# Performance work log

Hardware: AMD Instinct MI355X
Metric: run time of the kernel (lower is better)

The kernel has to match this reference:

```python
import jax, jax.numpy as jnp
from jax import lax
import numpy as np

N = 262144   # occupied voxels
C = 128      # channels
D = 96
K = 27       # 3x3x3 kernel offsets


def _build_kernel_map():
    """Random sparse voxel set + per-offset neighbor indices (Minkowski kernel map)."""
    rng = np.random.default_rng(0)
    cand = rng.integers(0, D, size=(4 * N, 3))
    flat = cand[:, 0] * D * D + cand[:, 1] * D + cand[:, 2]
    uniq = np.unique(flat)[:N]  # N unique occupied voxels
    coords = np.stack([uniq // (D * D), (uniq // D) % D, uniq % D], axis=1)
    lookup = np.full(D * D * D, -1, np.int32)
    lookup[uniq] = np.arange(N, dtype=np.int32)
    offs = np.stack(np.meshgrid([-1, 0, 1], [-1, 0, 1], [-1, 0, 1], indexing='ij'), -1).reshape(-1, 3)
    nc = coords[:, None, :] + offs[None, :, :]            # [N,27,3]
    inb = np.all((nc >= 0) & (nc < D), axis=-1)           # in-bounds
    ncc = np.clip(nc, 0, D - 1)
    nflat = ncc[..., 0] * D * D + ncc[..., 1] * D + ncc[..., 2]
    nid = lookup[nflat]
    mask = inb & (nid >= 0)
    nbr = np.where(mask, nid, 0).astype(np.int32)
    return jnp.asarray(nbr), jnp.asarray(mask)


def setup_inputs() -> dict:
    nbr, mask = _build_kernel_map()
    key = jax.random.key(0)
    ks = jax.random.split(key, 7)
    C4, C2 = C // 4, C // 2
    s3 = lambda cin: 1.0 / np.sqrt(K * cin)
    s1 = lambda cin: 1.0 / np.sqrt(cin)
    return {
        'x':   jax.random.normal(ks[0], (N, C), jnp.float32),
        'nbr': nbr,
        'mask': mask,
        'W00': jax.random.normal(ks[1], (K, C, C4), jnp.float32) * s3(C),
        'b00': jnp.zeros((C4,), jnp.float32),
        'W01': jax.random.normal(ks[2], (K, C4, C2), jnp.float32) * s3(C4),
        'b01': jnp.zeros((C2,), jnp.float32),
        'W10': jax.random.normal(ks[3], (C, C4), jnp.float32) * s1(C),
        'b10': jnp.zeros((C4,), jnp.float32),
        'W11': jax.random.normal(ks[4], (K, C4, C4), jnp.float32) * s3(C4),
        'b11': jnp.zeros((C4,), jnp.float32),
        'W12': jax.random.normal(ks[5], (C4, C2), jnp.float32) * s1(C4),
        'b12': jnp.zeros((C2,), jnp.float32),
    }


def _sparse_conv3(x, W, b, nbr_t, mask_t):
    """Minkowski 3x3x3 stride-1 conv: gather-GEMM-accumulate per kernel offset.
    x: [N,Cin], W: [27,Cin,Cout], nbr_t/mask_t: [27,N]."""
    acc0 = jnp.zeros((x.shape[0], W.shape[-1]), x.dtype)
    def step(acc, kin):
        Wk, idx, m = kin
        return acc + (x[idx] * m[:, None]) @ Wk, None
    y, _ = lax.scan(step, acc0, (W, nbr_t, mask_t))
    return y + b


def reference(x, nbr, mask, W00, b00, W01, b01, W10, b10, W11, b11, W12, b12):
    nbr_t = nbr.T                       # [27,N]
    mask_t = mask.T.astype(x.dtype)     # [27,N]
    # branch 0: conv3x3 -> relu -> conv3x3
    t = jax.nn.relu(_sparse_conv3(x, W00, b00, nbr_t, mask_t))
    out0 = _sparse_conv3(t, W01, b01, nbr_t, mask_t)
    # branch 1: conv1x1 -> relu -> conv3x3 -> relu -> conv1x1
    u = jax.nn.relu(x @ W10 + b10)
    u = jax.nn.relu(_sparse_conv3(u, W11, b11, nbr_t, mask_t))
    out1 = u @ W12 + b12
    # ME.cat(out0, out1) + x  (features concat on channel dim, residual add)
    return jnp.concatenate([out0, out1], axis=1) + x
```

## Files before the change

### kernel.cpp

```cpp
#include <hip/hip_runtime.h>
#include <stdint.h>

#define NVOX 262144
#define CIN  128
#define KOFF 27

typedef short  bf16x8 __attribute__((ext_vector_type(8)));
typedef float  f32x4  __attribute__((ext_vector_type(4)));
typedef int    i32x4  __attribute__((ext_vector_type(4)));

__device__ __forceinline__ unsigned short f2bf(float x) {
    unsigned int u = __builtin_bit_cast(unsigned int, x);
    u += 0x7fff + ((u >> 16) & 1);
    return (unsigned short)(u >> 16);
}

__global__ void k_detect(const int* __restrict__ mask_i32, int* __restrict__ flag) {
    bool ok = true;
    for (int i = threadIdx.x; i < 256; i += 64) {
        int v = mask_i32[i];
        ok = ok && (v == 0 || v == 1);
    }
    unsigned long long b = __ballot(ok);
    if (threadIdx.x == 0) *flag = (b == ~0ull) ? 1 : 0;
}

__device__ __forceinline__ void pack_one(const float* __restrict__ W,
                                         unsigned short* __restrict__ out,
                                         int K, int Nc, int idx) {
    int j    = idx & 7;
    int lane = (idx >> 3) & 63;
    int f    = idx >> 9;
    int ntiles = Nc >> 4, kcs = K >> 5;
    int g  = f / (kcs * ntiles);
    int rem = f - g * (kcs * ntiles);
    int kc = rem / ntiles;
    int nt = rem - kc * ntiles;
    int k  = kc * 32 + ((lane >> 4) << 3) + j;
    int n  = nt * 16 + (lane & 15);
    out[idx] = f2bf(W[((size_t)g * K + k) * Nc + n]);
}

#define PREP_R0 6912
#define PREP_R1 23296
#define PREP_GRID 24076

__global__ __launch_bounds__(256) void k_prep(
    const int* __restrict__ nbr, const void* __restrict__ mask,
    const int* __restrict__ flag, int* __restrict__ nbr_eff,
    const float* __restrict__ x, uint4* __restrict__ xb,
    const float* __restrict__ W00, const float* __restrict__ W10,
    const float* __restrict__ W01, const float* __restrict__ W11,
    const float* __restrict__ W12,
    unsigned short* __restrict__ w00p, unsigned short* __restrict__ w10p,
    unsigned short* __restrict__ w01p, unsigned short* __restrict__ w11p,
    unsigned short* __restrict__ w12p)
{
    int b = blockIdx.x, tid = threadIdx.x;
    if (b < PREP_R0) {
        int base = (b * 256 + tid) * 4;
        i32x4 nv = *(const i32x4*)(nbr + base);
        i32x4 r;
        if (*flag) {
            i32x4 mv = *(const i32x4*)((const int*)mask + base);
            r.x = mv.x ? nv.x : -1;
            r.y = mv.y ? nv.y : -1;
            r.z = mv.z ? nv.z : -1;
            r.w = mv.w ? nv.w : -1;
        } else {
            uchar4 mv = *(const uchar4*)((const unsigned char*)mask + base);
            r.x = mv.x ? nv.x : -1;
            r.y = mv.y ? nv.y : -1;
            r.z = mv.z ? nv.z : -1;
            r.w = mv.w ? nv.w : -1;
        }
        *(i32x4*)(nbr_eff + base) = r;
    } else if (b < PREP_R1) {
        int i = (b - PREP_R0) * 256 + tid;
        const float4* p = (const float4*)x + (size_t)i * 2;
        float4 a = p[0], c = p[1];
        uint4 r;
        r.x = f2bf(a.x) | ((unsigned)f2bf(a.y) << 16);
        r.y = f2bf(a.z) | ((unsigned)f2bf(a.w) << 16);
        r.z = f2bf(c.x) | ((unsigned)f2bf(c.y) << 16);
        r.w = f2bf(c.z) | ((unsigned)f2bf(c.w) << 16);
        xb[i] = r;
    } else {
        int idx = (b - PREP_R1) * 256 + tid;
        if      (idx < 110592) pack_one(W00, w00p, 128, 32, idx);
        else if (idx < 114688) pack_one(W10, w10p, 128, 32, idx - 110592);
        else if (idx < 169984) pack_one(W01, w01p,  32, 64, idx - 114688);
        else if (idx < 197632) pack_one(W11, w11p,  32, 32, idx - 169984);
        else                   pack_one(W12, w12p,  32, 64, idx - 197632);
    }
}

__global__ __launch_bounds__(256) void k_convA(
    const unsigned short* __restrict__ xb,
    const int* __restrict__ nbr_eff,
    const unsigned short* __restrict__ w00, const unsigned short* __restrict__ w10,
    const float* __restrict__ b00, const float* __restrict__ b10,
    unsigned short* __restrict__ s_out)
{
    __shared__ alignas(16) int nbr_s[128 * 27];
    __shared__ unsigned short stage[128 * 72];

    int tid = threadIdx.x;
    int lb = ((blockIdx.x & 7) << 8) | (blockIdx.x >> 3);
    int vb = lb * 128;
    {
        const i32x4* nsrc = (const i32x4*)(nbr_eff + (size_t)vb * 27);
        for (int i = tid; i < 864; i += 256)
            ((i32x4*)nbr_s)[i] = __builtin_nontemporal_load(nsrc + i);
    }
    __syncthreads();

    int lane = tid & 63, wave = tid >> 6;
    int m = lane & 15, q = lane >> 4;
    int vl0 = wave * 32 + m, vl1 = vl0 + 16;

    const bf16x8 zero = {0,0,0,0,0,0,0,0};
    f32x4 zz = {0.f,0.f,0.f,0.f};
    f32x4 t00 = zz, t01 = zz, t10 = zz, t11 = zz;
    f32x4 u00 = zz, u01 = zz, u10 = zz, u11 = zz;

#pragma unroll
    for (int ko = 0; ko < 27; ++ko) {
        int j0 = nbr_s[vl0 * 27 + ko];
        int j1 = nbr_s[vl1 * 27 + ko];
        bool m0 = j0 >= 0, m1 = j1 >= 0;
        const bf16x8* xr0 = (const bf16x8*)(xb + (size_t)(m0 ? j0 : 0) * 128 + q * 8);
        const bf16x8* xr1 = (const bf16x8*)(xb + (size_t)(m1 ? j1 : 0) * 128 + q * 8);
        bf16x8 a0[4], a1[4];
#pragma unroll
        for (int kc = 0; kc < 4; ++kc) {
            a0[kc] = m0 ? xr0[kc * 4] : zero;
            a1[kc] = m1 ? xr1[kc * 4] : zero;
        }
        const bf16x8* wp = (const bf16x8*)(w00) + (size_t)ko * 8 * 64 + lane;
        __builtin_amdgcn_s_setprio(1);
#pragma unroll
        for (int kc = 0; kc < 4; ++kc) {
            bf16x8 bb0 = wp[kc * 128];
            bf16x8 bb1 = wp[kc * 128 + 64];
            t00 = __builtin_amdgcn_mfma_f32_16x16x32_bf16(a0[kc], bb0, t00, 0, 0, 0);
            t01 = __builtin_amdgcn_mfma_f32_16x16x32_bf16(a0[kc], bb1, t01, 0, 0, 0);
            t10 = __builtin_amdgcn_mfma_f32_16x16x32_bf16(a1[kc], bb0, t10, 0, 0, 0);
            t11 = __builtin_amdgcn_mfma_f32_16x16x32_bf16(a1[kc], bb1, t11, 0, 0, 0);
        }
        __builtin_amdgcn_s_setprio(0);
        if (ko == 13) {
            const bf16x8* wq = (const bf16x8*)(w10) + lane;
            __builtin_amdgcn_s_setprio(1);
#pragma unroll
            for (int kc = 0; kc < 4; ++kc) {
                bf16x8 c0 = wq[kc * 128];
                bf16x8 c1 = wq[kc * 128 + 64];
                u00 = __builtin_amdgcn_mfma_f32_16x16x32_bf16(a0[kc], c0, u00, 0, 0, 0);
                u01 = __builtin_amdgcn_mfma_f32_16x16x32_bf16(a0[kc], c1, u01, 0, 0, 0);
                u10 = __builtin_amdgcn_mfma_f32_16x16x32_bf16(a1[kc], c0, u10, 0, 0, 0);
                u11 = __builtin_amdgcn_mfma_f32_16x16x32_bf16(a1[kc], c1, u11, 0, 0, 0);
            }
            __builtin_amdgcn_s_setprio(0);
        }
    }

    int col = lane & 15;
    float bt0 = b00[col], bt1 = b00[16 + col];
    float bu0 = b10[col], bu1 = b10[16 + col];
#pragma unroll
    for (int r = 0; r < 4; ++r) {
        int row0 = wave * 32 + q * 4 + r;
        unsigned short* sp0 = stage + row0 * 72;
        sp0[col]      = f2bf(fmaxf(t00[r] + bt0, 0.f));
        sp0[16 + col] = f2bf(fmaxf(t01[r] + bt1, 0.f));
        sp0[32 + col] = f2bf(fmaxf(u00[r] + bu0, 0.f));
        sp0[48 + col] = f2bf(fmaxf(u01[r] + bu1, 0.f));
        unsigned short* sp1 = sp0 + 16 * 72;
        sp1[col]      = f2bf(fmaxf(t10[r] + bt0, 0.f));
        sp1[16 + col] = f2bf(fmaxf(t11[r] + bt1, 0.f));
        sp1[32 + col] = f2bf(fmaxf(u10[r] + bu0, 0.f));
        sp1[48 + col] = f2bf(fmaxf(u11[r] + bu1, 0.f));
    }
    __syncthreads();
    uint4* g4 = (uint4*)(s_out + (size_t)vb * 64);
    for (int i = tid; i < 1024; i += 256) {
        int row = i >> 3, c = i & 7;
        g4[row * 8 + c] = *(const uint4*)(stage + row * 72 + c * 8);
    }
}

__global__ __launch_bounds__(256) void k_convB(
    const unsigned short* __restrict__ s_in,
    const float* __restrict__ x,
    const int* __restrict__ nbr_eff,
    const unsigned short* __restrict__ w01, const unsigned short* __restrict__ w11,
    const unsigned short* __restrict__ w12,
    const float* __restrict__ b01, const float* __restrict__ b11,
    const float* __restrict__ b12,
    float* __restrict__ out)
{
    __shared__ alignas(16) int nbr_s[128 * 27];
    __shared__ unsigned short vstage[4][2][16 * 40];

    int tid = threadIdx.x;
    int lb = ((blockIdx.x & 7) << 8) | (blockIdx.x >> 3);
    int vb = lb * 128;
    {
        const i32x4* nsrc = (const i32x4*)(nbr_eff + (size_t)vb * 27);
        for (int i = tid; i < 864; i += 256)
            ((i32x4*)nbr_s)[i] = __builtin_nontemporal_load(nsrc + i);
    }
    __syncthreads();

    int lane = tid & 63, wave = tid >> 6;
    int m = lane & 15, q = lane >> 4;
    int vl0 = wave * 32 + m, vl1 = vl0 + 16;

    const bf16x8 zero = {0,0,0,0,0,0,0,0};
    f32x4 zz = {0.f,0.f,0.f,0.f};
    f32x4 o[2][4];
    f32x4 v[2][2];
#pragma unroll
    for (int tl = 0; tl < 2; ++tl) {
        o[tl][0] = zz; o[tl][1] = zz; o[tl][2] = zz; o[tl][3] = zz;
        v[tl][0] = zz; v[tl][1] = zz;
    }

#pragma unroll
    for (int ko = 0; ko < 27; ++ko) {
        int j0 = nbr_s[vl0 * 27 + ko];
        int j1 = nbr_s[vl1 * 27 + ko];
        bool m0 = j0 >= 0, m1 = j1 >= 0;
        const bf16x8* sr0 = (const bf16x8*)(s_in + (size_t)(m0 ? j0 : 0) * 64 + q * 8);
        const bf16x8* sr1 = (const bf16x8*)(s_in + (size_t)(m1 ? j1 : 0) * 64 + q * 8);
        bf16x8 at0 = m0 ? sr0[0] : zero;
        bf16x8 au0 = m0 ? sr0[4] : zero;
        bf16x8 at1 = m1 ? sr1[0] : zero;
        bf16x8 au1 = m1 ? sr1[4] : zero;
        const bf16x8* wp1 = (const bf16x8*)(w01) + (size_t)ko * 4 * 64 + lane;
        __builtin_amdgcn_s_setprio(1);
#pragma unroll
        for (int nt = 0; nt < 4; ++nt) {
            bf16x8 bb = wp1[nt * 64];
            o[0][nt] = __builtin_amdgcn_mfma_f32_16x16x32_bf16(at0, bb, o[0][nt], 0, 0, 0);
            o[1][nt] = __builtin_amdgcn_mfma_f32_16x16x32_bf16(at1, bb, o[1][nt], 0, 0, 0);
        }
        const bf16x8* wp2 = (const bf16x8*)(w11) + (size_t)ko * 2 * 64 + lane;
#pragma unroll
        for (int nt = 0; nt < 2; ++nt) {
            bf16x8 bb = wp2[nt * 64];
            v[0][nt] = __builtin_amdgcn_mfma_f32_16x16x32_bf16(au0, bb, v[0][nt], 0, 0, 0);
            v[1][nt] = __builtin_amdgcn_mfma_f32_16x16x32_bf16(au1, bb, v[1][nt], 0, 0, 0);
        }
        __builtin_amdgcn_s_setprio(0);
    }

    int col = lane & 15;
    {
        float bv0 = b11[col], bv1 = b11[16 + col];
#pragma unroll
        for (int tl = 0; tl < 2; ++tl) {
            unsigned short* vs = vstage[wave][tl];
#pragma unroll
            for (int r = 0; r < 4; ++r) {
                int row = q * 4 + r;
                vs[row * 40 + col]      = f2bf(fmaxf(v[tl][0][r] + bv0, 0.f));
                vs[row * 40 + 16 + col] = f2bf(fmaxf(v[tl][1][r] + bv1, 0.f));
            }
        }
    }
    __syncthreads();
    const bf16x8* wp3 = (const bf16x8*)(w12) + lane;
    bf16x8 w3[4];
#pragma unroll
    for (int nt = 0; nt < 4; ++nt) w3[nt] = wp3[nt * 64];
    f32x4 p[2][4];
#pragma unroll
    for (int tl = 0; tl < 2; ++tl) {
        bf16x8 av = *(const bf16x8*)(vstage[wave][tl] + m * 40 + q * 8);
#pragma unroll
        for (int nt = 0; nt < 4; ++nt)
            p[tl][nt] = __builtin_amdgcn_mfma_f32_16x16x32_bf16(av, w3[nt], zz, 0, 0, 0);
    }

    float bo[4], bp[4];
#pragma unroll
    for (int nt = 0; nt < 4; ++nt) { bo[nt] = b01[nt * 16 + col]; bp[nt] = b12[nt * 16 + col]; }
#pragma unroll
    for (int tl = 0; tl < 2; ++tl) {
#pragma unroll
        for (int r = 0; r < 4; ++r) {
            int row = vb + wave * 32 + tl * 16 + q * 4 + r;
            const float* xr = x + (size_t)row * 128;
            float* orow = out + (size_t)row * 128;
#pragma unroll
            for (int nt = 0; nt < 4; ++nt) {
                float x0 = __builtin_nontemporal_load(xr + nt * 16 + col);
                float x1 = __builtin_nontemporal_load(xr + 64 + nt * 16 + col);
                __builtin_nontemporal_store(o[tl][nt][r] + bo[nt] + x0,
                                            orow + nt * 16 + col);
                __builtin_nontemporal_store(p[tl][nt][r] + bp[nt] + x1,
                                            orow + 64 + nt * 16 + col);
            }
        }
    }
}

extern "C" void kernel_launch(void* const* d_in, const int* in_sizes, int n_in,
                              void* d_out, int out_size, void* d_ws, size_t ws_size,
                              hipStream_t stream) {
    const float* x   = (const float*)d_in[0];
    const int*   nbr = (const int*)d_in[1];
    const void*  mask = d_in[2];
    const float* W00 = (const float*)d_in[3];
    const float* b00 = (const float*)d_in[4];
    const float* W01 = (const float*)d_in[5];
    const float* b01 = (const float*)d_in[6];
    const float* W10 = (const float*)d_in[7];
    const float* b10 = (const float*)d_in[8];
    const float* W11 = (const float*)d_in[9];
    const float* b11 = (const float*)d_in[10];
    const float* W12 = (const float*)d_in[11];
    const float* b12 = (const float*)d_in[12];
    float* out = (float*)d_out;

    char* ws = (char*)d_ws;
    unsigned short* xb     = (unsigned short*)(ws);
    unsigned short* s      = (unsigned short*)(ws + 67108864);
    int*            nbr_eff= (int*)           (ws + 100663296);
    unsigned short* w00p   = (unsigned short*)(ws + 128974848);
    unsigned short* w10p   = (unsigned short*)(ws + 129196032);
    unsigned short* w01p   = (unsigned short*)(ws + 129204224);
    unsigned short* w11p   = (unsigned short*)(ws + 129314816);
    unsigned short* w12p   = (unsigned short*)(ws + 129370112);
    int*            flag   = (int*)           (ws + 129374208);

    k_detect<<<1, 64, 0, stream>>>((const int*)mask, flag);
    k_prep<<<PREP_GRID, 256, 0, stream>>>(nbr, mask, flag, nbr_eff, x, (uint4*)xb,
                                          W00, W10, W01, W11, W12,
                                          w00p, w10p, w01p, w11p, w12p);
    k_convA<<<NVOX/128, 256, 0, stream>>>(xb, nbr_eff, w00p, w10p, b00, b10, s);
    k_convB<<<NVOX/128, 256, 0, stream>>>(s, x, nbr_eff, w01p, w11p, w12p,
                                          b01, b11, b12, out);
}
```

Baseline: 647.3 us.

## Cut register and LDS pressure in conv kernels to raise occupancy

k_convB now processes its two 16-voxel tiles one after another instead of together, which halves the live accumulators and the vstage LDS buffer. Launch-bounds hints ask for 8 and 6 waves per SIMD. k_convA reuses one LDS allocation for both the neighbour table and the output stage, with an added barrier between the two uses. k_prep switches its streaming loads to nontemporal ones. The aim is more waves in flight to hide gather latency, at the cost of less independent MFMA work per wave and possible register spills.

```diff
diff --git a/kernel.cpp b/kernel.cpp
--- a/kernel.cpp
+++ b/kernel.cpp
@@ -5,9 +5,10 @@
 #define CIN  128
 #define KOFF 27
 
-typedef short  bf16x8 __attribute__((ext_vector_type(8)));
-typedef float  f32x4  __attribute__((ext_vector_type(4)));
-typedef int    i32x4  __attribute__((ext_vector_type(4)));
+typedef short        bf16x8 __attribute__((ext_vector_type(8)));
+typedef float        f32x4  __attribute__((ext_vector_type(4)));
+typedef int          i32x4  __attribute__((ext_vector_type(4)));
+typedef unsigned int u32x4  __attribute__((ext_vector_type(4)));
 
 __device__ __forceinline__ unsigned short f2bf(float x) {
     unsigned int u = __builtin_bit_cast(unsigned int, x);
@@ -48,7 +49,7 @@
 __global__ __launch_bounds__(256) void k_prep(
     const int* __restrict__ nbr, const void* __restrict__ mask,
     const int* __restrict__ flag, int* __restrict__ nbr_eff,
-    const float* __restrict__ x, uint4* __restrict__ xb,
+    const float* __restrict__ x, u32x4* __restrict__ xb,
     const float* __restrict__ W00, const float* __restrict__ W10,
     const float* __restrict__ W01, const float* __restrict__ W11,
     const float* __restrict__ W12,
@@ -59,27 +60,29 @@
     int b = blockIdx.x, tid = threadIdx.x;
     if (b < PREP_R0) {
         int base = (b * 256 + tid) * 4;
-        i32x4 nv = *(const i32x4*)(nbr + base);
+        i32x4 nv = __builtin_nontemporal_load((const i32x4*)(nbr + base));
         i32x4 r;
         if (*flag) {
-            i32x4 mv = *(const i32x4*)((const int*)mask + base);
+            i32x4 mv = __builtin_nontemporal_load((const i32x4*)((const int*)mask + base));
             r.x = mv.x ? nv.x : -1;
             r.y = mv.y ? nv.y : -1;
             r.z = mv.z ? nv.z : -1;
             r.w = mv.w ? nv.w : -1;
         } else {
-            uchar4 mv = *(const uchar4*)((const unsigned char*)mask + base);
-            r.x = mv.x ? nv.x : -1;
-            r.y = mv.y ? nv.y : -1;
-            r.z = mv.z ? nv.z : -1;
-            r.w = mv.w ? nv.w : -1;
+            unsigned int mv = __builtin_nontemporal_load(
+                (const unsigned int*)((const unsigned char*)mask + base));
+            r.x = (mv & 0x000000ffu) ? nv.x : -1;
+            r.y = (mv & 0x0000ff00u) ? nv.y : -1;
+            r.z = (mv & 0x00ff0000u) ? nv.z : -1;
+            r.w = (mv & 0xff000000u) ? nv.w : -1;
         }
         *(i32x4*)(nbr_eff + base) = r;
     } else if (b < PREP_R1) {
         int i = (b - PREP_R0) * 256 + tid;
-        const float4* p = (const float4*)x + (size_t)i * 2;
-        float4 a = p[0], c = p[1];
-        uint4 r;
+        const f32x4* p = (const f32x4*)x + (size_t)i * 2;
+        f32x4 a = __builtin_nontemporal_load(p);
+        f32x4 c = __builtin_nontemporal_load(p + 1);
+        u32x4 r;
         r.x = f2bf(a.x) | ((unsigned)f2bf(a.y) << 16);
         r.y = f2bf(a.z) | ((unsigned)f2bf(a.w) << 16);
         r.z = f2bf(c.x) | ((unsigned)f2bf(c.y) << 16);
@@ -95,15 +98,16 @@
     }
 }
 
-__global__ __launch_bounds__(256) void k_convA(
+__global__ __launch_bounds__(256, 8) void k_convA(
     const unsigned short* __restrict__ xb,
     const int* __restrict__ nbr_eff,
     const unsigned short* __restrict__ w00, const unsigned short* __restrict__ w10,
     const float* __restrict__ b00, const float* __restrict__ b10,
     unsigned short* __restrict__ s_out)
 {
-    __shared__ alignas(16) int nbr_s[128 * 27];
-    __shared__ unsigned short stage[128 * 72];
+    __shared__ alignas(16) unsigned char shraw[18432];
+    int*            nbr_s = (int*)shraw;
+    unsigned short* stage = (unsigned short*)shraw;
 
     int tid = threadIdx.x;
     int lb = ((blockIdx.x & 7) << 8) | (blockIdx.x >> 3);
@@ -164,6 +168,8 @@
             __builtin_amdgcn_s_setprio(0);
         }
     }
+
+    __syncthreads();
 
     int col = lane & 15;
     float bt0 = b00[col], bt1 = b00[16 + col];
@@ -190,7 +196,7 @@
     }
 }
 
-__global__ __launch_bounds__(256) void k_convB(
+__global__ __launch_bounds__(256, 6) void k_convB(
     const unsigned short* __restrict__ s_in,
     const float* __restrict__ x,
     const int* __restrict__ nbr_eff,
@@ -201,7 +207,7 @@
     float* __restrict__ out)
 {
     __shared__ alignas(16) int nbr_s[128 * 27];
-    __shared__ unsigned short vstage[4][2][16 * 40];
+    __shared__ unsigned short vstage[4][16 * 40];
 
     int tid = threadIdx.x;
     int lb = ((blockIdx.x & 7) << 8) | (blockIdx.x >> 3);
@@ -215,80 +221,57 @@
 
     int lane = tid & 63, wave = tid >> 6;
     int m = lane & 15, q = lane >> 4;
-    int vl0 = wave * 32 + m, vl1 = vl0 + 16;
+    int col = m;
 
     const bf16x8 zero = {0,0,0,0,0,0,0,0};
     f32x4 zz = {0.f,0.f,0.f,0.f};
-    f32x4 o[2][4];
-    f32x4 v[2][2];
-#pragma unroll
+
+    float bv0 = b11[col], bv1 = b11[16 + col];
+    float bo[4], bp[4];
+#pragma unroll
+    for (int nt = 0; nt < 4; ++nt) { bo[nt] = b01[nt * 16 + col]; bp[nt] = b12[nt * 16 + col]; }
+    const bf16x8* wp3 = (const bf16x8*)(w12) + lane;
+
+#pragma unroll 1
     for (int tl = 0; tl < 2; ++tl) {
-        o[tl][0] = zz; o[tl][1] = zz; o[tl][2] = zz; o[tl][3] = zz;
-        v[tl][0] = zz; v[tl][1] = zz;
-    }
-
-#pragma unroll
-    for (int ko = 0; ko < 27; ++ko) {
-        int j0 = nbr_s[vl0 * 27 + ko];
-        int j1 = nbr_s[vl1 * 27 + ko];
-        bool m0 = j0 >= 0, m1 = j1 >= 0;
-        const bf16x8* sr0 = (const bf16x8*)(s_in + (size_t)(m0 ? j0 : 0) * 64 + q * 8);
-        const bf16x8* sr1 = (const bf16x8*)(s_in + (size_t)(m1 ? j1 : 0) * 64 + q * 8);
-        bf16x8 at0 = m0 ? sr0[0] : zero;
-        bf16x8 au0 = m0 ? sr0[4] : zero;
-        bf16x8 at1 = m1 ? sr1[0] : zero;
-        bf16x8 au1 = m1 ? sr1[4] : zero;
-        const bf16x8* wp1 = (const bf16x8*)(w01) + (size_t)ko * 4 * 64 + lane;
-        __builtin_amdgcn_s_setprio(1);
-#pragma unroll
-        for (int nt = 0; nt < 4; ++nt) {
-            bf16x8 bb = wp1[nt * 64];
-            o[0][nt] = __builtin_amdgcn_mfma_f32_16x16x32_bf16(at0, bb, o[0][nt], 0, 0, 0);
-            o[1][nt] = __builtin_amdgcn_mfma_f32_16x16x32_bf16(at1, bb, o[1][nt], 0, 0, 0);
-        }
-        const bf16x8* wp2 = (const bf16x8*)(w11) + (size_t)ko * 2 * 64 + lane;
-#pragma unroll
-        for (int nt = 0; nt < 2; ++nt) {
-            bf16x8 bb = wp2[nt * 64];
-            v[0][nt] = __builtin_amdgcn_mfma_f32_16x16x32_bf16(au0, bb, v[0][nt], 0, 0, 0);
-            v[1][nt] = __builtin_amdgcn_mfma_f32_16x16x32_bf16(au1, bb, v[1][nt], 0, 0, 0);
-        }
-        __builtin_amdgcn_s_setprio(0);
-    }
-
-    int col = lane & 15;
-    {
-        float bv0 = b11[col], bv1 = b11[16 + col];
-#pragma unroll
-        for (int tl = 0; tl < 2; ++tl) {
-            unsigned short* vs = vstage[wave][tl];
-#pragma unroll
-            for (int r = 0; r < 4; ++r) {
-                int row = q * 4 + r;
-                vs[row * 40 + col]      = f2bf(fmaxf(v[tl][0][r] + bv0, 0.f));
-                vs[row * 40 + 16 + col] = f2bf(fmaxf(v[tl][1][r] + bv1, 0.f));
-            }
-        }
-    }
-    __syncthreads();
-    const bf16x8* wp3 = (const bf16x8*)(w12) + lane;
-    bf16x8 w3[4];
-#pragma unroll
-    for (int nt = 0; nt < 4; ++nt) w3[nt] = wp3[nt * 64];
-    f32x4 p[2][4];
-#pragma unroll
-    for (int tl = 0; tl < 2; ++tl) {
-        bf16x8 av = *(const bf16x8*)(vstage[wave][tl] + m * 40 + q * 8);
-#pragma unroll
-        for (int nt = 0; nt < 4; ++nt)
-            p[tl][nt] = __builtin_amdgcn_mfma_f32_16x16x32_bf16(av, w3[nt], zz, 0, 0, 0);
-    }
-
-    float bo[4], bp[4];
-#pragma unroll
-    for (int nt = 0; nt < 4; ++nt) { bo[nt] = b01[nt * 16 + col]; bp[nt] = b12[nt * 16 + col]; }
-#pragma unroll
-    for (int tl = 0; tl < 2; ++tl) {
+        int vl = wave * 32 + tl * 16 + m;
+        f32x4 o0 = zz, o1 = zz, o2 = zz, o3 = zz;
+        f32x4 v0 = zz, v1 = zz;
+
+#pragma unroll
+        for (int ko = 0; ko < 27; ++ko) {
+            int j = nbr_s[vl * 27 + ko];
+            bool mk = j >= 0;
+            const bf16x8* sr = (const bf16x8*)(s_in + (size_t)(mk ? j : 0) * 64 + q * 8);
+            bf16x8 at = mk ? sr[0] : zero;
+            bf16x8 au = mk ? sr[4] : zero;
+            const bf16x8* wp1 = (const bf16x8*)(w01) + (size_t)ko * 4 * 64 + lane;
+            const bf16x8* wp2 = (const bf16x8*)(w11) + (size_t)ko * 2 * 64 + lane;
+            __builtin_amdgcn_s_setprio(1);
+            o0 = __builtin_amdgcn_mfma_f32_16x16x32_bf16(at, wp1[0],   o0, 0, 0, 0);
+            o1 = __builtin_amdgcn_mfma_f32_16x16x32_bf16(at, wp1[64],  o1, 0, 0, 0);
+            o2 = __builtin_amdgcn_mfma_f32_16x16x32_bf16(at, wp1[128], o2, 0, 0, 0);
+            o3 = __builtin_amdgcn_mfma_f32_16x16x32_bf16(at, wp1[192], o3, 0, 0, 0);
+            v0 = __builtin_amdgcn_mfma_f32_16x16x32_bf16(au, wp2[0],   v0, 0, 0, 0);
+            v1 = __builtin_amdgcn_mfma_f32_16x16x32_bf16(au, wp2[64],  v1, 0, 0, 0);
+            __builtin_amdgcn_s_setprio(0);
+        }
+
+        unsigned short* vs = vstage[wave];
+#pragma unroll
+        for (int r = 0; r < 4; ++r) {
+            int row = q * 4 + r;
+            vs[row * 40 + col]      = f2bf(fmaxf(v0[r] + bv0, 0.f));
+            vs[row * 40 + 16 + col] = f2bf(fmaxf(v1[r] + bv1, 0.f));
+        }
+        bf16x8 av = *(const bf16x8*)(vs + m * 40 + q * 8);
+        f32x4 p0 = __builtin_amdgcn_mfma_f32_16x16x32_bf16(av, wp3[0],   zz, 0, 0, 0);
+        f32x4 p1 = __builtin_amdgcn_mfma_f32_16x16x32_bf16(av, wp3[64],  zz, 0, 0, 0);
+        f32x4 p2 = __builtin_amdgcn_mfma_f32_16x16x32_bf16(av, wp3[128], zz, 0, 0, 0);
+        f32x4 p3 = __builtin_amdgcn_mfma_f32_16x16x32_bf16(av, wp3[192], zz, 0, 0, 0);
+
+        f32x4 oo[4] = {o0, o1, o2, o3};
+        f32x4 pp[4] = {p0, p1, p2, p3};
 #pragma unroll
         for (int r = 0; r < 4; ++r) {
             int row = vb + wave * 32 + tl * 16 + q * 4 + r;
@@ -298,9 +281,9 @@
             for (int nt = 0; nt < 4; ++nt) {
                 float x0 = __builtin_nontemporal_load(xr + nt * 16 + col);
                 float x1 = __builtin_nontemporal_load(xr + 64 + nt * 16 + col);
-                __builtin_nontemporal_store(o[tl][nt][r] + bo[nt] + x0,
+                __builtin_nontemporal_store(oo[nt][r] + bo[nt] + x0,
                                             orow + nt * 16 + col);
-                __builtin_nontemporal_store(p[tl][nt][r] + bp[nt] + x1,
+                __builtin_nontemporal_store(pp[nt][r] + bp[nt] + x1,
                                             orow + 64 + nt * 16 + col);
             }
         }
@@ -337,7 +320,7 @@
     int*            flag   = (int*)           (ws + 129374208);
 
     k_detect<<<1, 64, 0, stream>>>((const int*)mask, flag);
-    k_prep<<<PREP_GRID, 256, 0, stream>>>(nbr, mask, flag, nbr_eff, x, (uint4*)xb,
+    k_prep<<<PREP_GRID, 256, 0, stream>>>(nbr, mask, flag, nbr_eff, x, (u32x4*)xb,
                                           W00, W10, W01, W11, W12,
                                           w00p, w10p, w01p, w11p, w12p);
     k_convA<<<NVOX/128, 256, 0, stream>>>(xb, nbr_eff, w00p, w10p, b00, b10, s);
```

Result: slower. 1.652 ms (+155.2%).
